# Performance work log

Measured on AMD Instinct MI355X. Metric: run time of the kernel, lower is better.

Reference implementation:

```python
import math
import jax, jax.numpy as jnp
import numpy as np
from jax import lax

B, T, D = 2, 2048, 1024
H, W, E = 16, 16, 8
HD = D // H


def setup_inputs() -> dict:
    key = jax.random.key(0)
    ks = jax.random.split(key, 9)
    s = 0.02
    return {
        "x": jax.random.normal(ks[0], (B, T, D), dtype=jnp.float32),
        # CausalConv1d weights: torch Conv1d layout [out_ch, in_ch, kernel]
        "q_w": jax.random.normal(ks[1], (D, D, W), dtype=jnp.float32) * s,
        "q_b": jax.random.normal(ks[2], (D,), dtype=jnp.float32) * s,
        "k_w": jax.random.normal(ks[3], (D, D, W), dtype=jnp.float32) * s,
        "k_b": jax.random.normal(ks[4], (D,), dtype=jnp.float32) * s,
        # Linear weights: torch layout [out, in]
        "v_w": jax.random.normal(ks[5], (D, D), dtype=jnp.float32) * s,
        "v_b": jax.random.normal(ks[6], (D,), dtype=jnp.float32) * s,
        "p_w": jax.random.normal(ks[7], (D, D), dtype=jnp.float32) * s,
        "p_b": jax.random.normal(ks[8], (D,), dtype=jnp.float32) * s,
    }


def _causal_conv(x_t, w, b):
    # x_t: [B, D, T]; left-pad by W-1 so output at t sees inputs <= t
    xp = jnp.pad(x_t, ((0, 0), (0, 0), (W - 1, 0)))
    y = lax.conv_general_dilated(xp, w, window_strides=(1,), padding="VALID",
                                 dimension_numbers=("NCH", "OIH", "NCH"))
    return y + b[None, :, None]


def _split_heads(z):
    # [B, T, D] -> [B, H, T, hd]
    return z.reshape(B, T, H, HD).transpose(0, 2, 1, 3)


def reference(x, q_w, q_b, k_w, k_b, v_w, v_b, p_w, p_b):
    x_t = x.transpose(0, 2, 1)  # [B, D, T]
    q = _split_heads(_causal_conv(x_t, q_w, q_b).transpose(0, 2, 1))
    k = _split_heads(_causal_conv(x_t, k_w, k_b).transpose(0, 2, 1))
    v = _split_heads(jnp.einsum("btd,od->bto", x, v_w) + v_b)
    scale = 1.0 / math.sqrt(HD)

    # ---- local window attention (unfold equivalent) ----
    # zero-pad keys/values W-1 steps to the left along T, gather sliding windows
    k_pad = jnp.pad(k, ((0, 0), (0, 0), (W - 1, 0), (0, 0)))
    v_pad = jnp.pad(v, ((0, 0), (0, 0), (W - 1, 0), (0, 0)))
    widx = jnp.arange(T)[:, None] + jnp.arange(W)[None, :]  # [T, W]
    patches_k = k_pad[:, :, widx]  # [B, H, T, W, hd]
    patches_v = v_pad[:, :, widx]  # [B, H, T, W, hd]
    attn_l = jax.nn.softmax(jnp.einsum("bhtd,bhtwd->bhtw", q, patches_k) * scale, axis=-1)
    out_l = jnp.einsum("bhtw,bhtwd->bhtd", attn_l, patches_v)

    # ---- exponential jumps: roll by 2^e (wrap-around, as in original) ----
    out_e = jnp.zeros_like(out_l)
    for e in range(E):
        shift = 2 ** e
        if shift >= T:
            break
        k_s = jnp.roll(k, -shift, axis=2)
        v_s = jnp.roll(v, -shift, axis=2)
        score = jnp.sum(q * k_s, axis=-1) * scale  # [B, H, T]
        alpha = jax.nn.softmax(score, axis=-1)[..., None]  # softmax over T (faithful)
        out_e = out_e + alpha * v_s

    out = (out_l + out_e).transpose(0, 2, 1, 3).reshape(B, T, D)
    return jnp.einsum("btd,od->bto", out, p_w) + p_b
```

## Files before the change

kernel.cpp:

```cpp
#include <hip/hip_runtime.h>
#include <cstdint>
#include <cstddef>

#define TSEQ 2048
#define DDIM 1024

typedef _Float16 f16;
typedef _Float16 f16x4 __attribute__((ext_vector_type(4)));
typedef _Float16 f16x8 __attribute__((ext_vector_type(8)));
typedef float f32x4 __attribute__((ext_vector_type(4)));

__device__ __align__(16) static const unsigned char g_zero16[16] = {};

__device__ __forceinline__ void gload_lds16(const void* g, void* l) {
  __builtin_amdgcn_global_load_lds(
      (const __attribute__((address_space(1))) void*)g,
      (__attribute__((address_space(3))) void*)l, 16, 0, 0);
}

__global__ void cvt_f32_f16(const float* __restrict__ src, f16* __restrict__ dst, int n4) {
  int i = blockIdx.x * 256 + threadIdx.x;
  if (i >= n4) return;
  float4 v = ((const float4*)src)[i];
  f16x4 h = { (f16)v.x, (f16)v.y, (f16)v.z, (f16)v.w };
  ((f16x4*)dst)[i] = h;
}

__global__ void cvt_w_transpose(const float* __restrict__ qw, const float* __restrict__ kw,
                                f16* __restrict__ qwh, f16* __restrict__ kwh) {
  __shared__ float tile[64 * 17];
  int o = blockIdx.x;
  const float* src;
  f16* dst;
  if (o < 1024) { src = qw + (size_t)o * 16384; dst = qwh + (size_t)o * 16384; }
  else          { src = kw + (size_t)(o - 1024) * 16384; dst = kwh + (size_t)(o - 1024) * 16384; }
  for (int i0 = 0; i0 < 1024; i0 += 64) {
    __syncthreads();
    #pragma unroll
    for (int p = 0; p < 4; p++) {
      int idx = p * 256 + threadIdx.x;
      float v = src[i0 * 16 + idx];
      tile[(idx >> 4) * 17 + (idx & 15)] = v;
    }
    __syncthreads();
    #pragma unroll
    for (int p = 0; p < 4; p++) {
      int idx = p * 256 + threadIdx.x;
      int w = idx >> 6, ii = idx & 63;
      dst[w * 1024 + i0 + ii] = (f16)tile[ii * 17 + w];
    }
  }
}

__global__ __launch_bounds__(256, 2) void gemm_qk(
    const f16* __restrict__ xh,
    const f16* __restrict__ Bq, const f16* __restrict__ Bk,
    const float* __restrict__ bq, const float* __restrict__ bk,
    f16* __restrict__ oq, f16* __restrict__ ok)
{
  __shared__ __align__(16) f16 smem[16384];
  const int tid = threadIdx.x;
  const int lane = tid & 63;
  const int wid = tid >> 6;
  const int wm = wid & 1;
  const int ks = wid >> 1;

  const int m0 = blockIdx.x * 128;
  const int n0 = blockIdx.y * 64;
  const int bT = m0 & ~(TSEQ - 1);
  const int t0 = m0 & (TSEQ - 1);

  const int srow = lane >> 3;
  const int scg = ((lane & 7) ^ ((lane >> 3) & 7)) * 8;

  f32x4 accq[4][4] = {};
  f32x4 acck[4][4] = {};

  const int slotoff = (((ks * 4 + (lane >> 4)) ^ (lane & 7)) * 8);

  for (int kk = 0; kk < 16384; kk += 64) {
    __syncthreads();
    if (wid < 2) {
      const int w = kk >> 10;
      const int i0 = (kk & (DDIM - 1)) + scg;
      #pragma unroll
      for (int c = 0; c < 8; c++) {
        const int s = wid * 8 + c;
        const int r = s * 8 + srow;
        const int srcT = t0 + r + w - 15;
        const void* g = (srcT >= 0)
            ? (const void*)(xh + (((size_t)(bT + srcT)) << 10) + i0)
            : (const void*)g_zero16;
        gload_lds16(g, (void*)&smem[s * 512]);
      }
    } else if (wid == 2) {
      #pragma unroll
      for (int c = 0; c < 8; c++) {
        const int r = c * 8 + srow;
        const void* g = (const void*)(Bq + ((size_t)(n0 + r) << 14) + kk + scg);
        gload_lds16(g, (void*)&smem[8192 + c * 512]);
      }
    } else {
      #pragma unroll
      for (int c = 0; c < 8; c++) {
        const int r = c * 8 + srow;
        const void* g = (const void*)(Bk + ((size_t)(n0 + r) << 14) + kk + scg);
        gload_lds16(g, (void*)&smem[12288 + c * 512]);
      }
    }
    __syncthreads();

    f16x8 af[4], bfq[4], bfk[4];
    #pragma unroll
    for (int i = 0; i < 4; i++) {
      const int r = wm * 64 + i * 16 + (lane & 15);
      af[i] = *(const f16x8*)&smem[r * 64 + slotoff];
    }
    #pragma unroll
    for (int j = 0; j < 4; j++) {
      const int r = j * 16 + (lane & 15);
      bfq[j] = *(const f16x8*)&smem[8192 + r * 64 + slotoff];
      bfk[j] = *(const f16x8*)&smem[12288 + r * 64 + slotoff];
    }
    #pragma unroll
    for (int i = 0; i < 4; i++)
      #pragma unroll
      for (int j = 0; j < 4; j++) {
        accq[i][j] = __builtin_amdgcn_mfma_f32_16x16x32_f16(af[i], bfq[j], accq[i][j], 0, 0, 0);
        acck[i][j] = __builtin_amdgcn_mfma_f32_16x16x32_f16(af[i], bfk[j], acck[i][j], 0, 0, 0);
      }
  }

  const int crow = (lane >> 4) * 4;
  const int ccol = lane & 15;
  float* red = (float*)smem + wm * 4096;

  __syncthreads();
  if (ks == 1) {
    #pragma unroll
    for (int i = 0; i < 4; i++)
      #pragma unroll
      for (int j = 0; j < 4; j++)
        #pragma unroll
        for (int r = 0; r < 4; r++)
          red[(i * 16 + crow + r) * 64 + j * 16 + ccol] = accq[i][j][r];
  }
  __syncthreads();
  if (ks == 0) {
    #pragma unroll
    for (int j = 0; j < 4; j++) {
      const int col = n0 + j * 16 + ccol;
      const float bvl = bq[col];
      #pragma unroll
      for (int i = 0; i < 4; i++)
        #pragma unroll
        for (int r = 0; r < 4; r++) {
          const int row = m0 + wm * 64 + i * 16 + crow + r;
          const float v = accq[i][j][r] + red[(i * 16 + crow + r) * 64 + j * 16 + ccol] + bvl;
          oq[(size_t)row * DDIM + col] = (f16)v;
        }
    }
  }
  __syncthreads();
  if (ks == 1) {
    #pragma unroll
    for (int i = 0; i < 4; i++)
      #pragma unroll
      for (int j = 0; j < 4; j++)
        #pragma unroll
        for (int r = 0; r < 4; r++)
          red[(i * 16 + crow + r) * 64 + j * 16 + ccol] = acck[i][j][r];
  }
  __syncthreads();
  if (ks == 0) {
    #pragma unroll
    for (int j = 0; j < 4; j++) {
      const int col = n0 + j * 16 + ccol;
      const float bvl = bk[col];
      #pragma unroll
      for (int i = 0; i < 4; i++)
        #pragma unroll
        for (int r = 0; r < 4; r++) {
          const int row = m0 + wm * 64 + i * 16 + crow + r;
          const float v = acck[i][j][r] + red[(i * 16 + crow + r) * 64 + j * 16 + ccol] + bvl;
          ok[(size_t)row * DDIM + col] = (f16)v;
        }
    }
  }
}

template<int MODE>
__global__ __launch_bounds__(256, 2) void gemm_small(
    const f16* __restrict__ A, const f16* __restrict__ Bw,
    const float* __restrict__ bias, f16* __restrict__ oh, float* __restrict__ ofp)
{
  __shared__ f16 As[128 * 32];
  __shared__ f16 Bs[128 * 32];
  const int tid = threadIdx.x;
  const int lane = tid & 63;
  const int wid = tid >> 6;
  const int m0 = blockIdx.x * 128;
  const int n0 = blockIdx.y * 128;

  const int srow = lane >> 2;
  const int scg = ((lane & 3) ^ ((lane >> 3) & 3)) * 8;
  const int wm = wid & 1;
  const int wn = wid >> 1;

  f32x4 acc[4][4] = {};

  for (int kk = 0; kk < 1024; kk += 32) {
    __syncthreads();
    if (wid < 2) {
      #pragma unroll
      for (int c = 0; c < 4; c++) {
        const int r = wid * 64 + c * 16 + srow;
        const void* g = (const void*)(A + (((size_t)(m0 + r)) << 10) + kk + scg);
        gload_lds16(g, (void*)&As[(wid * 64 + c * 16) * 32]);
      }
    } else {
      #pragma unroll
      for (int c = 0; c < 4; c++) {
        const int r = (wid - 2) * 64 + c * 16 + srow;
        const void* g = (const void*)(Bw + (((size_t)(n0 + r)) << 10) + kk + scg);
        gload_lds16(g, (void*)&Bs[((wid - 2) * 64 + c * 16) * 32]);
      }
    }
    __syncthreads();
    const int koff = ((lane >> 4) ^ ((lane >> 1) & 3)) * 8;
    f16x8 af[4], bf[4];
    #pragma unroll
    for (int i = 0; i < 4; i++) {
      af[i] = *(const f16x8*)&As[(wm * 64 + i * 16 + (lane & 15)) * 32 + koff];
      bf[i] = *(const f16x8*)&Bs[(wn * 64 + i * 16 + (lane & 15)) * 32 + koff];
    }
    #pragma unroll
    for (int i = 0; i < 4; i++)
      #pragma unroll
      for (int j = 0; j < 4; j++)
        acc[i][j] = __builtin_amdgcn_mfma_f32_16x16x32_f16(af[i], bf[j], acc[i][j], 0, 0, 0);
  }

  const int crow = (lane >> 4) * 4;
  const int ccol = lane & 15;
  #pragma unroll
  for (int j = 0; j < 4; j++) {
    const int col = n0 + wn * 64 + j * 16 + ccol;
    const float bvl = bias[col];
    #pragma unroll
    for (int i = 0; i < 4; i++) {
      #pragma unroll
      for (int r = 0; r < 4; r++) {
        const int row = m0 + wm * 64 + i * 16 + crow + r;
        const float val = acc[i][j][r] + bvl;
        if (MODE == 1) ofp[(size_t)row * DDIM + col] = val;
        else           oh[(size_t)row * DDIM + col] = (f16)val;
      }
    }
  }
}

__global__ void score_k(const f16* __restrict__ qh, const f16* __restrict__ kh,
                        float* __restrict__ scores) {
  int bid = blockIdx.x;
  int bh = bid >> 3, tc = bid & 7;
  int b = bh >> 4, h = bh & 15;
  int t = tc * 256 + threadIdx.x;
  const f16* qrow = qh + (((size_t)(b * TSEQ + t)) << 10) + h * 64;
  float qv[64];
  #pragma unroll
  for (int c = 0; c < 8; c++) {
    f16x8 v = *(const f16x8*)(qrow + c * 8);
    #pragma unroll
    for (int j = 0; j < 8; j++) qv[c * 8 + j] = (float)v[j];
  }
  #pragma unroll
  for (int e = 0; e < 8; e++) {
    int ts = t + (1 << e);
    if (ts >= TSEQ) ts -= TSEQ;
    const f16* krow = kh + (((size_t)(b * TSEQ + ts)) << 10) + h * 64;
    float s = 0.f;
    #pragma unroll
    for (int c = 0; c < 8; c++) {
      f16x8 v = *(const f16x8*)(krow + c * 8);
      #pragma unroll
      for (int j = 0; j < 8; j++) s += qv[c * 8 + j] * (float)v[j];
    }
    scores[((size_t)(bh * 8 + e) << 11) + t] = s * 0.125f;
  }
}

__global__ void softmax_k(float* __restrict__ scores) {
  __shared__ float red[4];
  int row = blockIdx.x;
  float* p = scores + ((size_t)row << 11);
  int tid = threadIdx.x;
  float v[8];
  float4 a = ((const float4*)p)[tid * 2];
  float4 b = ((const float4*)p)[tid * 2 + 1];
  v[0] = a.x; v[1] = a.y; v[2] = a.z; v[3] = a.w;
  v[4] = b.x; v[5] = b.y; v[6] = b.z; v[7] = b.w;
  float m = v[0];
  #pragma unroll
  for (int j = 1; j < 8; j++) m = fmaxf(m, v[j]);
  for (int o = 32; o > 0; o >>= 1) m = fmaxf(m, __shfl_xor(m, o, 64));
  if ((tid & 63) == 0) red[tid >> 6] = m;
  __syncthreads();
  m = fmaxf(fmaxf(red[0], red[1]), fmaxf(red[2], red[3]));
  __syncthreads();
  float s = 0.f;
  #pragma unroll
  for (int j = 0; j < 8; j++) { v[j] = __expf(v[j] - m); s += v[j]; }
  for (int o = 32; o > 0; o >>= 1) s += __shfl_xor(s, o, 64);
  if ((tid & 63) == 0) red[tid >> 6] = s;
  __syncthreads();
  s = (red[0] + red[1]) + (red[2] + red[3]);
  float inv = 1.0f / s;
  float4 o1 = make_float4(v[0] * inv, v[1] * inv, v[2] * inv, v[3] * inv);
  float4 o2 = make_float4(v[4] * inv, v[5] * inv, v[6] * inv, v[7] * inv);
  ((float4*)p)[tid * 2] = o1;
  ((float4*)p)[tid * 2 + 1] = o2;
}

__global__ __launch_bounds__(256) void attn_out_k(
    const f16* __restrict__ qh, const f16* __restrict__ kh, const f16* __restrict__ vh,
    const float* __restrict__ alpha, f16* __restrict__ outh)
{
  __shared__ f16 qL[128 * 64];
  __shared__ f16 vL[271 * 64];
  __shared__ float scL[128 * 16];
  __shared__ float aL[8 * 128];
  const int bh = blockIdx.x, tc = blockIdx.y;
  const int b = bh >> 4, h = bh & 15;
  const int t0 = tc * 128;
  const int tid = threadIdx.x;
  const size_t base = (((size_t)(b * TSEQ)) << 10) + h * 64;

  for (int idx = tid; idx < 128 * 8; idx += 256) {
    int r = idx >> 3, c = idx & 7;
    *(uint4*)&qL[r * 64 + c * 8] = *(const uint4*)(qh + base + (((size_t)(t0 + r)) << 10) + c * 8);
  }
  for (int idx = tid; idx < 271 * 8; idx += 256) {
    int j = idx >> 3, c = idx & 7;
    int r = t0 - 15 + j;
    uint4 val;
    if (r < 0) val = make_uint4(0, 0, 0, 0);
    else {
      int rr = (r >= TSEQ) ? r - TSEQ : r;
      val = *(const uint4*)(vh + base + (((size_t)rr) << 10) + c * 8);
    }
    *(uint4*)&vL[j * 64 + c * 8] = val;
  }
  {
    int e = tid >> 5, t4 = (tid & 31) * 4;
    *(float4*)&aL[e * 128 + t4] =
        *(const float4*)(alpha + ((size_t)(bh * 8 + e) << 11) + t0 + t4);
  }
  __syncthreads();

  {
    const int tl = tid & 127;
    const int wg = tid >> 7;
    float qv[64];
    #pragma unroll
    for (int c = 0; c < 8; c++) {
      f16x8 v = *(const f16x8*)&qL[tl * 64 + c * 8];
      #pragma unroll
      for (int j = 0; j < 8; j++) qv[c * 8 + j] = (float)v[j];
    }
    #pragma unroll
    for (int wi = 0; wi < 8; wi++) {
      const int w = wg * 8 + wi;
      const int r = t0 + tl - 15 + w;
      float s = 0.f;
      if (r >= 0) {
        const f16* kr = kh + base + (((size_t)r) << 10);
        #pragma unroll
        for (int c = 0; c < 8; c++) {
          f16x8 v = *(const f16x8*)(kr + c * 8);
          #pragma unroll
          for (int j = 0; j < 8; j++) s += qv[c * 8 + j] * (float)v[j];
        }
      }
      scL[tl * 16 + w] = s * 0.125f;
    }
  }
  __syncthreads();

  if (tid < 128) {
    float sc[16];
    float m = -1e30f;
    #pragma unroll
    for (int w = 0; w < 16; w++) { sc[w] = scL[tid * 16 + w]; m = fmaxf(m, sc[w]); }
    float sum = 0.f;
    #pragma unroll
    for (int w = 0; w < 16; w++) { sc[w] = __expf(sc[w] - m); sum += sc[w]; }
    float inv = 1.0f / sum;
    #pragma unroll
    for (int w = 0; w < 16; w++) scL[tid * 16 + w] = sc[w] * inv;
  }
  __syncthreads();

  {
    const int tl = tid >> 1;
    const int d0 = (tid & 1) * 32;
    float accv[32] = {};
    #pragma unroll
    for (int w = 0; w < 16; w++) {
      const float pw_ = scL[tl * 16 + w];
      const f16* vr = &vL[(tl + w) * 64 + d0];
      #pragma unroll
      for (int c = 0; c < 4; c++) {
        f16x8 v = *(const f16x8*)(vr + c * 8);
        #pragma unroll
        for (int j = 0; j < 8; j++) accv[c * 8 + j] += pw_ * (float)v[j];
      }
    }
    #pragma unroll
    for (int e = 0; e < 8; e++) {
      const float a = aL[e * 128 + tl];
      const f16* vr = &vL[(tl + 15 + (1 << e)) * 64 + d0];
      #pragma unroll
      for (int c = 0; c < 4; c++) {
        f16x8 v = *(const f16x8*)(vr + c * 8);
        #pragma unroll
        for (int j = 0; j < 8; j++) accv[c * 8 + j] += a * (float)v[j];
      }
    }
    f16* orow = outh + base + (((size_t)(t0 + tl)) << 10) + d0;
    #pragma unroll
    for (int c = 0; c < 4; c++) {
      f16x8 v;
      #pragma unroll
      for (int j = 0; j < 8; j++) v[j] = (f16)accv[c * 8 + j];
      *(f16x8*)(orow + c * 8) = v;
    }
  }
}

extern "C" void kernel_launch(void* const* d_in, const int* in_sizes, int n_in,
                              void* d_out, int out_size, void* d_ws, size_t ws_size,
                              hipStream_t stream) {
  (void)in_sizes; (void)n_in; (void)out_size; (void)ws_size;
  const float* x   = (const float*)d_in[0];
  const float* q_w = (const float*)d_in[1];
  const float* q_b = (const float*)d_in[2];
  const float* k_w = (const float*)d_in[3];
  const float* k_b = (const float*)d_in[4];
  const float* v_w = (const float*)d_in[5];
  const float* v_b = (const float*)d_in[6];
  const float* p_w = (const float*)d_in[7];
  const float* p_b = (const float*)d_in[8];
  float* out = (float*)d_out;

  char* ws = (char*)d_ws;
  f16* xh      = (f16*)(ws);
  f16* qwh     = (f16*)(ws + 8388608);
  f16* kwh     = (f16*)(ws + 41943040);
  f16* vwh     = (f16*)(ws + 75497472);
  f16* pwh     = (f16*)(ws + 77594624);
  f16* qh      = (f16*)(ws + 79691776);
  f16* kh      = (f16*)(ws + 88080384);
  f16* vh      = (f16*)(ws + 96468992);
  f16* outh    = (f16*)(ws + 104857600);
  float* alpha = (float*)(ws + 113246208);

  cvt_f32_f16<<<4096, 256, 0, stream>>>(x, xh, 1048576);
  cvt_f32_f16<<<1024, 256, 0, stream>>>(v_w, vwh, 262144);
  cvt_f32_f16<<<1024, 256, 0, stream>>>(p_w, pwh, 262144);
  cvt_w_transpose<<<2048, 256, 0, stream>>>(q_w, k_w, qwh, kwh);

  gemm_qk<<<dim3(32, 16), 256, 0, stream>>>(xh, qwh, kwh, q_b, k_b, qh, kh);
  gemm_small<0><<<dim3(32, 8), 256, 0, stream>>>(xh, vwh, v_b, vh, nullptr);

  score_k<<<256, 256, 0, stream>>>(qh, kh, alpha);
  softmax_k<<<256, 256, 0, stream>>>(alpha);
  attn_out_k<<<dim3(32, 16), 256, 0, stream>>>(qh, kh, vh, alpha, outh);

  gemm_small<1><<<dim3(32, 8), 256, 0, stream>>>(outh, pwh, p_b, nullptr, out);
}
```

Before: 561.3 us.

## Double-buffer conv GEMM, store Q/K/V head-major, rework score and attention kernels

The conv GEMM now double-buffers its LDS stages so the next K-slice's global-to-LDS load is issued while the current slice is being consumed. GEMM epilogues write Q, K and V in a head-major [B,H,T,64] layout instead of [B,T,D]. score_k is rewritten to use 8-lane cooperative dot products with fdot2 and shuffles. attn_out_k uses 64-row tiles, a swizzled LDS K tile and fdot2, and launches twice as many blocks. Together these target latency stalls in the main GEMM and uncoalesced strided accesses in the attention kernels, at the cost of doubled LDS in gemm_qk (which may lower occupancy) and scattered 2-byte stores in the epilogues.

```diff
diff --git a/kernel.cpp b/kernel.cpp
--- a/kernel.cpp
+++ b/kernel.cpp
@@ -6,9 +6,11 @@
 #define DDIM 1024
 
 typedef _Float16 f16;
+typedef _Float16 f16x2 __attribute__((ext_vector_type(2)));
 typedef _Float16 f16x4 __attribute__((ext_vector_type(4)));
 typedef _Float16 f16x8 __attribute__((ext_vector_type(8)));
 typedef float f32x4 __attribute__((ext_vector_type(4)));
+
 
 __device__ __align__(16) static const unsigned char g_zero16[16] = {};
 
@@ -58,7 +60,7 @@
     const float* __restrict__ bq, const float* __restrict__ bk,
     f16* __restrict__ oq, f16* __restrict__ ok)
 {
-  __shared__ __align__(16) f16 smem[16384];
+  __shared__ __align__(16) f16 smem[32768];
   const int tid = threadIdx.x;
   const int lane = tid & 63;
   const int wid = tid >> 6;
@@ -78,8 +80,8 @@
 
   const int slotoff = (((ks * 4 + (lane >> 4)) ^ (lane & 7)) * 8);
 
-  for (int kk = 0; kk < 16384; kk += 64) {
-    __syncthreads();
+  auto stage = [&](int kk, int buf) {
+    f16* sb = &smem[buf * 16384];
     if (wid < 2) {
       const int w = kk >> 10;
       const int i0 = (kk & (DDIM - 1)) + scg;
@@ -91,36 +93,43 @@
         const void* g = (srcT >= 0)
             ? (const void*)(xh + (((size_t)(bT + srcT)) << 10) + i0)
             : (const void*)g_zero16;
-        gload_lds16(g, (void*)&smem[s * 512]);
+        gload_lds16(g, (void*)&sb[s * 512]);
       }
     } else if (wid == 2) {
       #pragma unroll
       for (int c = 0; c < 8; c++) {
         const int r = c * 8 + srow;
         const void* g = (const void*)(Bq + ((size_t)(n0 + r) << 14) + kk + scg);
-        gload_lds16(g, (void*)&smem[8192 + c * 512]);
+        gload_lds16(g, (void*)&sb[8192 + c * 512]);
       }
     } else {
       #pragma unroll
       for (int c = 0; c < 8; c++) {
         const int r = c * 8 + srow;
         const void* g = (const void*)(Bk + ((size_t)(n0 + r) << 14) + kk + scg);
-        gload_lds16(g, (void*)&smem[12288 + c * 512]);
-      }
-    }
+        gload_lds16(g, (void*)&sb[12288 + c * 512]);
+      }
+    }
+  };
+
+  stage(0, 0);
+  for (int kk = 0; kk < 16384; kk += 64) {
+    const int buf = (kk >> 6) & 1;
     __syncthreads();
-
+    if (kk + 64 < 16384) stage(kk + 64, buf ^ 1);
+
+    const f16* sb = &smem[buf * 16384];
     f16x8 af[4], bfq[4], bfk[4];
     #pragma unroll
     for (int i = 0; i < 4; i++) {
       const int r = wm * 64 + i * 16 + (lane & 15);
-      af[i] = *(const f16x8*)&smem[r * 64 + slotoff];
+      af[i] = *(const f16x8*)&sb[r * 64 + slotoff];
     }
     #pragma unroll
     for (int j = 0; j < 4; j++) {
       const int r = j * 16 + (lane & 15);
-      bfq[j] = *(const f16x8*)&smem[8192 + r * 64 + slotoff];
-      bfk[j] = *(const f16x8*)&smem[12288 + r * 64 + slotoff];
+      bfq[j] = *(const f16x8*)&sb[8192 + r * 64 + slotoff];
+      bfk[j] = *(const f16x8*)&sb[12288 + r * 64 + slotoff];
     }
     #pragma unroll
     for (int i = 0; i < 4; i++)
@@ -133,6 +142,7 @@
 
   const int crow = (lane >> 4) * 4;
   const int ccol = lane & 15;
+  const int hh = n0 >> 6;
   float* red = (float*)smem + wm * 4096;
 
   __syncthreads();
@@ -151,13 +161,15 @@
     for (int j = 0; j < 4; j++) {
       const int col = n0 + j * 16 + ccol;
       const float bvl = bq[col];
+      const int d = j * 16 + ccol;
       #pragma unroll
       for (int i = 0; i < 4; i++)
         #pragma unroll
         for (int r = 0; r < 4; r++) {
           const int row = m0 + wm * 64 + i * 16 + crow + r;
+          const int b = row >> 11, t = row & (TSEQ - 1);
           const float v = accq[i][j][r] + red[(i * 16 + crow + r) * 64 + j * 16 + ccol] + bvl;
-          oq[(size_t)row * DDIM + col] = (f16)v;
+          oq[((size_t)(b * 16 + hh) * TSEQ + t) * 64 + d] = (f16)v;
         }
     }
   }
@@ -177,13 +189,15 @@
     for (int j = 0; j < 4; j++) {
       const int col = n0 + j * 16 + ccol;
       const float bvl = bk[col];
+      const int d = j * 16 + ccol;
       #pragma unroll
       for (int i = 0; i < 4; i++)
         #pragma unroll
         for (int r = 0; r < 4; r++) {
           const int row = m0 + wm * 64 + i * 16 + crow + r;
+          const int b = row >> 11, t = row & (TSEQ - 1);
           const float v = acck[i][j][r] + red[(i * 16 + crow + r) * 64 + j * 16 + ccol] + bvl;
-          ok[(size_t)row * DDIM + col] = (f16)v;
+          ok[((size_t)(b * 16 + hh) * TSEQ + t) * 64 + d] = (f16)v;
         }
     }
   }
@@ -253,40 +267,48 @@
       for (int r = 0; r < 4; r++) {
         const int row = m0 + wm * 64 + i * 16 + crow + r;
         const float val = acc[i][j][r] + bvl;
-        if (MODE == 1) ofp[(size_t)row * DDIM + col] = val;
-        else           oh[(size_t)row * DDIM + col] = (f16)val;
-      }
-    }
-  }
-}
-
-__global__ void score_k(const f16* __restrict__ qh, const f16* __restrict__ kh,
-                        float* __restrict__ scores) {
-  int bid = blockIdx.x;
-  int bh = bid >> 3, tc = bid & 7;
-  int b = bh >> 4, h = bh & 15;
-  int t = tc * 256 + threadIdx.x;
-  const f16* qrow = qh + (((size_t)(b * TSEQ + t)) << 10) + h * 64;
-  float qv[64];
+        if (MODE == 1) {
+          ofp[(size_t)row * DDIM + col] = val;
+        } else {
+          const int b = row >> 11, t = row & (TSEQ - 1);
+          const int h = col >> 6, d = col & 63;
+          oh[((size_t)(b * 16 + h) * TSEQ + t) * 64 + d] = (f16)val;
+        }
+      }
+    }
+  }
+}
+
+__global__ __launch_bounds__(256) void score_k(const f16* __restrict__ qh,
+                                               const f16* __restrict__ kh,
+                                               float* __restrict__ scores) {
+  const int bid = blockIdx.x;
+  const int bh = bid >> 3, tc = bid & 7;
+  const int tid = threadIdx.x;
+  const int wave = tid >> 6, lane = tid & 63;
+  const int tr = lane >> 3, dc = lane & 7;
+  const size_t base = ((size_t)bh) << 17;
+  const f16* qb = qh + base;
+  const f16* kb = kh + base;
+
   #pragma unroll
-  for (int c = 0; c < 8; c++) {
-    f16x8 v = *(const f16x8*)(qrow + c * 8);
-    #pragma unroll
-    for (int j = 0; j < 8; j++) qv[c * 8 + j] = (float)v[j];
-  }
-  #pragma unroll
-  for (int e = 0; e < 8; e++) {
-    int ts = t + (1 << e);
-    if (ts >= TSEQ) ts -= TSEQ;
-    const f16* krow = kh + (((size_t)(b * TSEQ + ts)) << 10) + h * 64;
-    float s = 0.f;
-    #pragma unroll
-    for (int c = 0; c < 8; c++) {
-      f16x8 v = *(const f16x8*)(krow + c * 8);
-      #pragma unroll
-      for (int j = 0; j < 8; j++) s += qv[c * 8 + j] * (float)v[j];
-    }
-    scores[((size_t)(bh * 8 + e) << 11) + t] = s * 0.125f;
+  for (int p = 0; p < 8; p++) {
+    const int t = tc * 256 + wave * 64 + p * 8 + tr;
+    f16x8 qv = *(const f16x8*)(qb + (size_t)t * 64 + dc * 8);
+    const f16x2* qp = (const f16x2*)&qv;
+    #pragma unroll
+    for (int e = 0; e < 8; e++) {
+      const int ts = (t + (1 << e)) & (TSEQ - 1);
+      f16x8 kv = *(const f16x8*)(kb + (size_t)ts * 64 + dc * 8);
+      const f16x2* kp = (const f16x2*)&kv;
+      float s = 0.f;
+      #pragma unroll
+      for (int j = 0; j < 4; j++) s = __builtin_amdgcn_fdot2(qp[j], kp[j], s, false);
+      s += __shfl_xor(s, 1, 64);
+      s += __shfl_xor(s, 2, 64);
+      s += __shfl_xor(s, 4, 64);
+      if (dc == 0) scores[((size_t)(bh * 8 + e) << 11) + t] = s * 0.125f;
+    }
   }
 }
 
@@ -326,68 +348,69 @@
     const f16* __restrict__ qh, const f16* __restrict__ kh, const f16* __restrict__ vh,
     const float* __restrict__ alpha, f16* __restrict__ outh)
 {
-  __shared__ f16 qL[128 * 64];
-  __shared__ f16 vL[271 * 64];
-  __shared__ float scL[128 * 16];
-  __shared__ float aL[8 * 128];
+  __shared__ f16 qL[64 * 64];
+  __shared__ f16 kL[80 * 64];
+  __shared__ f16 vL[208 * 64];
+  __shared__ float scL[64 * 16];
+  __shared__ float aL[8 * 64];
   const int bh = blockIdx.x, tc = blockIdx.y;
-  const int b = bh >> 4, h = bh & 15;
-  const int t0 = tc * 128;
+  const int t0 = tc * 64;
   const int tid = threadIdx.x;
-  const size_t base = (((size_t)(b * TSEQ)) << 10) + h * 64;
-
-  for (int idx = tid; idx < 128 * 8; idx += 256) {
-    int r = idx >> 3, c = idx & 7;
-    *(uint4*)&qL[r * 64 + c * 8] = *(const uint4*)(qh + base + (((size_t)(t0 + r)) << 10) + c * 8);
-  }
-  for (int idx = tid; idx < 271 * 8; idx += 256) {
-    int j = idx >> 3, c = idx & 7;
-    int r = t0 - 15 + j;
+  const size_t base = ((size_t)bh) << 17;
+
+  for (int idx = tid; idx < 64 * 8; idx += 256) {
+    int r = idx >> 3, c = idx & 7, sl = c ^ (r & 7);
+    *(uint4*)&qL[r * 64 + sl * 8] = *(const uint4*)(qh + base + (size_t)(t0 + r) * 64 + c * 8);
+  }
+  for (int idx = tid; idx < 79 * 8; idx += 256) {
+    int r = idx >> 3, c = idx & 7, sl = c ^ (r & 7);
+    int g = t0 - 15 + r;
+    uint4 val = (g < 0) ? make_uint4(0, 0, 0, 0)
+                        : *(const uint4*)(kh + base + (size_t)g * 64 + c * 8);
+    *(uint4*)&kL[r * 64 + sl * 8] = val;
+  }
+  for (int idx = tid; idx < 207 * 8; idx += 256) {
+    int r = idx >> 3, c = idx & 7, sl = c ^ (r & 7);
+    int g = t0 - 15 + r;
     uint4 val;
-    if (r < 0) val = make_uint4(0, 0, 0, 0);
+    if (g < 0) val = make_uint4(0, 0, 0, 0);
     else {
-      int rr = (r >= TSEQ) ? r - TSEQ : r;
-      val = *(const uint4*)(vh + base + (((size_t)rr) << 10) + c * 8);
-    }
-    *(uint4*)&vL[j * 64 + c * 8] = val;
-  }
+      if (g >= TSEQ) g -= TSEQ;
+      val = *(const uint4*)(vh + base + (size_t)g * 64 + c * 8);
+    }
+    *(uint4*)&vL[r * 64 + sl * 8] = val;
+  }
+  for (int idx = tid; idx < 512; idx += 256) {
+    int e = idx >> 6, i = idx & 63;
+    aL[e * 64 + i] = alpha[((size_t)(bh * 8 + e) << 11) + t0 + i];
+  }
+  __syncthreads();
+
   {
-    int e = tid >> 5, t4 = (tid & 31) * 4;
-    *(float4*)&aL[e * 128 + t4] =
-        *(const float4*)(alpha + ((size_t)(bh * 8 + e) << 11) + t0 + t4);
-  }
-  __syncthreads();
-
-  {
-    const int tl = tid & 127;
-    const int wg = tid >> 7;
-    float qv[64];
-    #pragma unroll
-    for (int c = 0; c < 8; c++) {
-      f16x8 v = *(const f16x8*)&qL[tl * 64 + c * 8];
-      #pragma unroll
-      for (int j = 0; j < 8; j++) qv[c * 8 + j] = (float)v[j];
-    }
-    #pragma unroll
-    for (int wi = 0; wi < 8; wi++) {
-      const int w = wg * 8 + wi;
-      const int r = t0 + tl - 15 + w;
+    const int tl = tid & 63;
+    const int wg = tid >> 6;
+    f16x8 qv[8];
+    #pragma unroll
+    for (int c = 0; c < 8; c++) qv[c] = *(const f16x8*)&qL[tl * 64 + ((c ^ (tl & 7)) * 8)];
+    const f16x2* qp = (const f16x2*)&qv[0];
+    #pragma unroll
+    for (int wi = 0; wi < 4; wi++) {
+      const int w = wg * 4 + wi;
+      const int r = tl + w;
       float s = 0.f;
-      if (r >= 0) {
-        const f16* kr = kh + base + (((size_t)r) << 10);
-        #pragma unroll
-        for (int c = 0; c < 8; c++) {
-          f16x8 v = *(const f16x8*)(kr + c * 8);
-          #pragma unroll
-          for (int j = 0; j < 8; j++) s += qv[c * 8 + j] * (float)v[j];
-        }
+      #pragma unroll
+      for (int c = 0; c < 8; c++) {
+        f16x8 kv = *(const f16x8*)&kL[r * 64 + ((c ^ (r & 7)) * 8)];
+        const f16x2* kp = (const f16x2*)&kv;
+        #pragma unroll
+        for (int j = 0; j < 4; j++) s = __builtin_amdgcn_fdot2(qp[c * 4 + j], kp[j], s, false);
       }
       scL[tl * 16 + w] = s * 0.125f;
     }
   }
   __syncthreads();
 
-  if (tid < 128) {
+  if (tid < 64) {
     float sc[16];
     float m = -1e30f;
     #pragma unroll
@@ -402,38 +425,41 @@
   __syncthreads();
 
   {
-    const int tl = tid >> 1;
-    const int d0 = (tid & 1) * 32;
-    float accv[32] = {};
+    const int tl = tid >> 2;
+    const int qd = tid & 3;
+    float accv[16] = {};
     #pragma unroll
     for (int w = 0; w < 16; w++) {
       const float pw_ = scL[tl * 16 + w];
-      const f16* vr = &vL[(tl + w) * 64 + d0];
-      #pragma unroll
-      for (int c = 0; c < 4; c++) {
-        f16x8 v = *(const f16x8*)(vr + c * 8);
-        #pragma unroll
-        for (int j = 0; j < 8; j++) accv[c * 8 + j] += pw_ * (float)v[j];
+      const int r = tl + w;
+      #pragma unroll
+      for (int c2 = 0; c2 < 2; c2++) {
+        const int c = qd * 2 + c2;
+        f16x8 v = *(const f16x8*)&vL[r * 64 + ((c ^ (r & 7)) * 8)];
+        #pragma unroll
+        for (int j = 0; j < 8; j++) accv[c2 * 8 + j] += pw_ * (float)v[j];
       }
     }
     #pragma unroll
     for (int e = 0; e < 8; e++) {
-      const float a = aL[e * 128 + tl];
-      const f16* vr = &vL[(tl + 15 + (1 << e)) * 64 + d0];
-      #pragma unroll
-      for (int c = 0; c < 4; c++) {
-        f16x8 v = *(const f16x8*)(vr + c * 8);
-        #pragma unroll
-        for (int j = 0; j < 8; j++) accv[c * 8 + j] += a * (float)v[j];
-      }
-    }
-    f16* orow = outh + base + (((size_t)(t0 + tl)) << 10) + d0;
-    #pragma unroll
-    for (int c = 0; c < 4; c++) {
+      const float a = aL[e * 64 + tl];
+      const int r = tl + 15 + (1 << e);
+      #pragma unroll
+      for (int c2 = 0; c2 < 2; c2++) {
+        const int c = qd * 2 + c2;
+        f16x8 v = *(const f16x8*)&vL[r * 64 + ((c ^ (r & 7)) * 8)];
+        #pragma unroll
+        for (int j = 0; j < 8; j++) accv[c2 * 8 + j] += a * (float)v[j];
+      }
+    }
+    const int b = bh >> 4, h = bh & 15;
+    f16* orow = outh + ((size_t)(b * TSEQ + t0 + tl)) * DDIM + h * 64 + qd * 16;
+    #pragma unroll
+    for (int c2 = 0; c2 < 2; c2++) {
       f16x8 v;
       #pragma unroll
-      for (int j = 0; j < 8; j++) v[j] = (f16)accv[c * 8 + j];
-      *(f16x8*)(orow + c * 8) = v;
+      for (int j = 0; j < 8; j++) v[j] = (f16)accv[c2 * 8 + j];
+      *(f16x8*)(orow + c2 * 8) = v;
     }
   }
 }
@@ -475,7 +501,7 @@
 
   score_k<<<256, 256, 0, stream>>>(qh, kh, alpha);
   softmax_k<<<256, 256, 0, stream>>>(alpha);
-  attn_out_k<<<dim3(32, 16), 256, 0, stream>>>(qh, kh, vh, alpha, outh);
+  attn_out_k<<<dim3(32, 32), 256, 0, stream>>>(qh, kh, vh, alpha, outh);
 
   gemm_small<1><<<dim3(32, 8), 256, 0, stream>>>(outh, pwh, p_b, nullptr, out);
 }
```

Result: faster. 546.1 us (-2.7%).
